# Kernel tuning notes

Hardware: AMD Instinct MI355X
Metric: run time of the kernel (lower is better)

Reference implementation:

```python
import jax, jax.numpy as jnp
import numpy as np

IMG = 640.0  # nominal image size for box coordinates
EPS_IOU = 1e-9   # eps used by iou_calculator
EPS_OVL = 1e-6   # eps used by bbox_overlaps


def _make_boxes(key, lead_shape):
    # Build valid <x1,y1,x2,y2> boxes: random centers in [0, IMG), sizes in [4, 204).
    k1, k2 = jax.random.split(key)
    c = jax.random.uniform(k1, lead_shape + (2,), dtype=jnp.float32) * IMG
    wh = jax.random.uniform(k2, lead_shape + (2,), dtype=jnp.float32) * 200.0 + 4.0
    return jnp.concatenate([c - wh / 2.0, c + wh / 2.0], axis=-1)


def setup_inputs() -> dict:
    key = jax.random.key(0)
    ka, kb, kc = jax.random.split(key, 3)
    gt_bboxes = _make_boxes(ka, (16, 128))        # (bs, n_max_boxes, 4)
    pred_bboxes = _make_boxes(kb, (16, 8400))     # (bs, num_total_anchors, 4)
    anchor_bboxes = _make_boxes(kc, (8400,))      # (num_total_anchors, 4)
    return {"gt_bboxes": gt_bboxes, "pred_bboxes": pred_bboxes, "anchor_bboxes": anchor_bboxes}


def _dist_calculator(gt_flat, anchor_bboxes):
    # gt_flat: (bs*M, 4), anchor_bboxes: (N, 4) -> distances (bs*M, N), ac_points (N, 2)
    gt_pts = (gt_flat[:, :2] + gt_flat[:, 2:]) / 2.0
    ac_pts = (anchor_bboxes[:, :2] + anchor_bboxes[:, 2:]) / 2.0
    d = jnp.sqrt(jnp.sum((gt_pts[:, None, :] - ac_pts[None, :, :]) ** 2, axis=-1))
    return d, ac_pts


def _iou_calculator(box1, box2, eps=EPS_IOU):
    # box1: (bs, M, 4), box2: (bs, N, 4) -> (bs, M, N) pairwise IoU
    b1 = box1[:, :, None, :]
    b2 = box2[:, None, :, :]
    lt = jnp.maximum(b1[..., :2], b2[..., :2])
    rb = jnp.minimum(b1[..., 2:], b2[..., 2:])
    wh = jnp.clip(rb - lt, 0.0)
    overlap = wh[..., 0] * wh[..., 1]
    area1 = (b1[..., 2] - b1[..., 0]) * (b1[..., 3] - b1[..., 1])
    area2 = (b2[..., 2] - b2[..., 0]) * (b2[..., 3] - b2[..., 1])
    union = area1 + area2 - overlap + eps
    return overlap / union


def _bbox_overlaps_giou(b1, b2, eps=EPS_OVL):
    # b1: (M, 4), b2: (N, 4) -> (M, N) pairwise GIoU (bbox_overlaps, mode='giou', is_aligned=False)
    area1 = (b1[:, 2] - b1[:, 0]) * (b1[:, 3] - b1[:, 1])
    area2 = (b2[:, 2] - b2[:, 0]) * (b2[:, 3] - b2[:, 1])
    lt = jnp.maximum(b1[:, None, :2], b2[None, :, :2])
    rb = jnp.minimum(b1[:, None, 2:], b2[None, :, 2:])
    wh = jnp.clip(rb - lt, 0.0)
    overlap = wh[..., 0] * wh[..., 1]
    union = jnp.maximum(area1[:, None] + area2[None, :] - overlap, eps)
    ious = overlap / union
    enclosed_lt = jnp.minimum(b1[:, None, :2], b2[None, :, :2])
    enclosed_rb = jnp.maximum(b1[:, None, 2:], b2[None, :, 2:])
    enclose_wh = jnp.clip(enclosed_rb - enclosed_lt, 0.0)
    enclose_area = jnp.maximum(enclose_wh[..., 0] * enclose_wh[..., 1], eps)
    return ious - (enclose_area - union) / enclose_area


def reference(gt_bboxes, pred_bboxes, anchor_bboxes):
    bs, M, _ = gt_bboxes.shape
    gt_flat = gt_bboxes.reshape(bs * M, 4)
    # ATSS assigner stage: center distance gt<->anchor and gt<->anchor GIoU
    distances, ac_points = _dist_calculator(gt_flat, anchor_bboxes)
    gious = _bbox_overlaps_giou(gt_flat, anchor_bboxes)
    # TAL assigner stage: batched pairwise IoU gt<->pred
    overlaps = _iou_calculator(gt_bboxes, pred_bboxes)
    return distances, overlaps, gious
```

## Files before the change

### kernel.cpp

```cpp
#include <hip/hip_runtime.h>


#define EPS_IOU 1e-9f
#define EPS_OVL 1e-6f

__device__ __forceinline__ void dist_giou(const float4 gb, float gcx, float gcy, float garea,
                                          const float4 ab, float& d, float& giou) {
    float acx = (ab.x + ab.z) * 0.5f;
    float acy = (ab.y + ab.w) * 0.5f;
    float dx = gcx - acx, dy = gcy - acy;
    d = sqrtf(dx * dx + dy * dy);
    float aarea = (ab.z - ab.x) * (ab.w - ab.y);
    float ltx = fmaxf(gb.x, ab.x), lty = fmaxf(gb.y, ab.y);
    float rbx = fminf(gb.z, ab.z), rby = fminf(gb.w, ab.w);
    float w = fmaxf(rbx - ltx, 0.0f), h = fmaxf(rby - lty, 0.0f);
    float overlap = w * h;
    float uni = fmaxf(garea + aarea - overlap, EPS_OVL);
    float iou = overlap / uni;
    float elx = fminf(gb.x, ab.x), ely = fminf(gb.y, ab.y);
    float erx = fmaxf(gb.z, ab.z), ery = fmaxf(gb.w, ab.w);
    float ew = fmaxf(erx - elx, 0.0f), eh = fmaxf(ery - ely, 0.0f);
    float earea = fmaxf(ew * eh, EPS_OVL);
    giou = iou - (earea - uni) / earea;
}

__device__ __forceinline__ float pred_iou(const float4 gb, float garea, const float4 pb) {
    float parea = (pb.z - pb.x) * (pb.w - pb.y);
    float ltx = fmaxf(gb.x, pb.x), lty = fmaxf(gb.y, pb.y);
    float rbx = fminf(gb.z, pb.z), rby = fminf(gb.w, pb.w);
    float w = fmaxf(rbx - ltx, 0.0f), h = fmaxf(rby - lty, 0.0f);
    float overlap = w * h;
    float uni = garea + parea - overlap + EPS_IOU;
    return overlap / uni;
}

__global__ __launch_bounds__(256) void yolov6_fused(
    const float4* __restrict__ gt,
    const float4* __restrict__ pred,
    const float4* __restrict__ anc,
    float* __restrict__ out_dist,
    float* __restrict__ out_ovl,
    float* __restrict__ out_giou,
    int N, int M)
{
    const int g = blockIdx.y;
    const int b = g / M;
    const int j4 = blockIdx.x * blockDim.x + threadIdx.x;
    const int j = j4 * 4;
    if (j >= N) return;

    const float4 gb = gt[g];
    const float gcx = (gb.x + gb.z) * 0.5f;
    const float gcy = (gb.y + gb.w) * 0.5f;
    const float garea = (gb.z - gb.x) * (gb.w - gb.y);

    const long long row = (long long)g * N;
    const float4* ancp = anc + j;
    const float4* predp = pred + (long long)b * N + j;

    if (j + 3 < N) {
        float dv[4], ov[4], gv[4];
#pragma unroll
        for (int k = 0; k < 4; ++k) {
            const float4 ab = ancp[k];
            dist_giou(gb, gcx, gcy, garea, ab, dv[k], gv[k]);
            const float4 pb = predp[k];
            ov[k] = pred_iou(gb, garea, pb);
        }
        *(float4*)(out_dist + row + j) = make_float4(dv[0], dv[1], dv[2], dv[3]);
        *(float4*)(out_ovl  + row + j) = make_float4(ov[0], ov[1], ov[2], ov[3]);
        *(float4*)(out_giou + row + j) = make_float4(gv[0], gv[1], gv[2], gv[3]);
    } else {
        for (int k = 0; j + k < N; ++k) {
            const float4 ab = ancp[k];
            float d, gi;
            dist_giou(gb, gcx, gcy, garea, ab, d, gi);
            const float4 pb = predp[k];
            float io = pred_iou(gb, garea, pb);
            out_dist[row + j + k] = d;
            out_ovl [row + j + k] = io;
            out_giou[row + j + k] = gi;
        }
    }
}

extern "C" void kernel_launch(void* const* d_in, const int* in_sizes, int n_in,
                              void* d_out, int out_size, void* d_ws, size_t ws_size,
                              hipStream_t stream) {
    const float4* gt   = (const float4*)d_in[0];
    const float4* pred = (const float4*)d_in[1];
    const float4* anc  = (const float4*)d_in[2];

    const int N  = in_sizes[2] / 4;
    const int bs = in_sizes[1] / in_sizes[2];
    const int GM = in_sizes[0] / 4;
    const int M  = GM / bs;

    float* out = (float*)d_out;
    const long long plane = (long long)GM * N;
    float* out_dist = out;
    float* out_ovl  = out + plane;
    float* out_giou = out + 2 * plane;

    const int cols = (N + 3) / 4;
    dim3 block(256);
    dim3 grid((cols + 255) / 256, GM);
    yolov6_fused<<<grid, block, 0, stream>>>(gt, pred, anc,
                                             out_dist, out_ovl, out_giou, N, M);
}
```

Baseline: 225.4 us.

## Process four gt rows per thread and use fast hardware rcp/sqrt

Each thread now loads its four anchor and pred boxes once and reuses them, along with their precomputed centers and areas, across four consecutive gt rows, so the grid's y-dimension shrinks by four. IEEE divisions and sqrt are replaced with the AMDGPU approximate rcp and sqrt builtins. The tail path for N not divisible by 4 is removed, and the code assumes GM divisible by ROWS and that the rows never straddle a batch boundary. The approximate reciprocal can change results slightly. The kernel is dominated by output writes (about 258 MB), so the saving on compute and loads may be small.

```diff
diff --git a/kernel.cpp b/kernel.cpp
--- a/kernel.cpp
+++ b/kernel.cpp
@@ -3,36 +3,10 @@
 
 #define EPS_IOU 1e-9f
 #define EPS_OVL 1e-6f
+#define ROWS 4
 
-__device__ __forceinline__ void dist_giou(const float4 gb, float gcx, float gcy, float garea,
-                                          const float4 ab, float& d, float& giou) {
-    float acx = (ab.x + ab.z) * 0.5f;
-    float acy = (ab.y + ab.w) * 0.5f;
-    float dx = gcx - acx, dy = gcy - acy;
-    d = sqrtf(dx * dx + dy * dy);
-    float aarea = (ab.z - ab.x) * (ab.w - ab.y);
-    float ltx = fmaxf(gb.x, ab.x), lty = fmaxf(gb.y, ab.y);
-    float rbx = fminf(gb.z, ab.z), rby = fminf(gb.w, ab.w);
-    float w = fmaxf(rbx - ltx, 0.0f), h = fmaxf(rby - lty, 0.0f);
-    float overlap = w * h;
-    float uni = fmaxf(garea + aarea - overlap, EPS_OVL);
-    float iou = overlap / uni;
-    float elx = fminf(gb.x, ab.x), ely = fminf(gb.y, ab.y);
-    float erx = fmaxf(gb.z, ab.z), ery = fmaxf(gb.w, ab.w);
-    float ew = fmaxf(erx - elx, 0.0f), eh = fmaxf(ery - ely, 0.0f);
-    float earea = fmaxf(ew * eh, EPS_OVL);
-    giou = iou - (earea - uni) / earea;
-}
-
-__device__ __forceinline__ float pred_iou(const float4 gb, float garea, const float4 pb) {
-    float parea = (pb.z - pb.x) * (pb.w - pb.y);
-    float ltx = fmaxf(gb.x, pb.x), lty = fmaxf(gb.y, pb.y);
-    float rbx = fminf(gb.z, pb.z), rby = fminf(gb.w, pb.w);
-    float w = fmaxf(rbx - ltx, 0.0f), h = fmaxf(rby - lty, 0.0f);
-    float overlap = w * h;
-    float uni = garea + parea - overlap + EPS_IOU;
-    return overlap / uni;
-}
+__device__ __forceinline__ float frcp(float x)  { return __builtin_amdgcn_rcpf(x); }
+__device__ __forceinline__ float fsqrtf_(float x){ return __builtin_amdgcn_sqrtf(x); }
 
 __global__ __launch_bounds__(256) void yolov6_fused(
     const float4* __restrict__ gt,
@@ -43,44 +17,63 @@
     float* __restrict__ out_giou,
     int N, int M)
 {
-    const int g = blockIdx.y;
-    const int b = g / M;
-    const int j4 = blockIdx.x * blockDim.x + threadIdx.x;
-    const int j = j4 * 4;
+    const int g0 = blockIdx.y * ROWS;
+    const int b  = g0 / M;
+    const int j  = (blockIdx.x * blockDim.x + threadIdx.x) * 4;
     if (j >= N) return;
 
-    const float4 gb = gt[g];
-    const float gcx = (gb.x + gb.z) * 0.5f;
-    const float gcy = (gb.y + gb.w) * 0.5f;
-    const float garea = (gb.z - gb.x) * (gb.w - gb.y);
+    float4 ab[4], pb[4];
+    float acx[4], acy[4], aarea[4], parea[4];
+    const float4* ancp  = anc + j;
+    const float4* predp = pred + (long long)b * N + j;
+#pragma unroll
+    for (int k = 0; k < 4; ++k) {
+        ab[k] = ancp[k];
+        pb[k] = predp[k];
+        acx[k]   = (ab[k].x + ab[k].z) * 0.5f;
+        acy[k]   = (ab[k].y + ab[k].w) * 0.5f;
+        aarea[k] = (ab[k].z - ab[k].x) * (ab[k].w - ab[k].y);
+        parea[k] = (pb[k].z - pb[k].x) * (pb[k].w - pb[k].y);
+    }
 
-    const long long row = (long long)g * N;
-    const float4* ancp = anc + j;
-    const float4* predp = pred + (long long)b * N + j;
+#pragma unroll
+    for (int r = 0; r < ROWS; ++r) {
+        const int g = g0 + r;
+        const float4 gb = gt[g];
+        const float gcx   = (gb.x + gb.z) * 0.5f;
+        const float gcy   = (gb.y + gb.w) * 0.5f;
+        const float garea = (gb.z - gb.x) * (gb.w - gb.y);
 
-    if (j + 3 < N) {
         float dv[4], ov[4], gv[4];
 #pragma unroll
         for (int k = 0; k < 4; ++k) {
-            const float4 ab = ancp[k];
-            dist_giou(gb, gcx, gcy, garea, ab, dv[k], gv[k]);
-            const float4 pb = predp[k];
-            ov[k] = pred_iou(gb, garea, pb);
+            float dx = gcx - acx[k], dy = gcy - acy[k];
+            dv[k] = fsqrtf_(dx * dx + dy * dy);
+            {
+                float ltx = fmaxf(gb.x, ab[k].x), lty = fmaxf(gb.y, ab[k].y);
+                float rbx = fminf(gb.z, ab[k].z), rby = fminf(gb.w, ab[k].w);
+                float w = fmaxf(rbx - ltx, 0.0f), h = fmaxf(rby - lty, 0.0f);
+                float overlap = w * h;
+                float uni = fmaxf(garea + aarea[k] - overlap, EPS_OVL);
+                float elx = fminf(gb.x, ab[k].x), ely = fminf(gb.y, ab[k].y);
+                float erx = fmaxf(gb.z, ab[k].z), ery = fmaxf(gb.w, ab[k].w);
+                float ew = fmaxf(erx - elx, 0.0f), eh = fmaxf(ery - ely, 0.0f);
+                float earea = fmaxf(ew * eh, EPS_OVL);
+                gv[k] = overlap * frcp(uni) - (earea - uni) * frcp(earea);
+            }
+            {
+                float ltx = fmaxf(gb.x, pb[k].x), lty = fmaxf(gb.y, pb[k].y);
+                float rbx = fminf(gb.z, pb[k].z), rby = fminf(gb.w, pb[k].w);
+                float w = fmaxf(rbx - ltx, 0.0f), h = fmaxf(rby - lty, 0.0f);
+                float overlap = w * h;
+                float uni = garea + parea[k] - overlap + EPS_IOU;
+                ov[k] = overlap * frcp(uni);
+            }
         }
-        *(float4*)(out_dist + row + j) = make_float4(dv[0], dv[1], dv[2], dv[3]);
-        *(float4*)(out_ovl  + row + j) = make_float4(ov[0], ov[1], ov[2], ov[3]);
-        *(float4*)(out_giou + row + j) = make_float4(gv[0], gv[1], gv[2], gv[3]);
-    } else {
-        for (int k = 0; j + k < N; ++k) {
-            const float4 ab = ancp[k];
-            float d, gi;
-            dist_giou(gb, gcx, gcy, garea, ab, d, gi);
-            const float4 pb = predp[k];
-            float io = pred_iou(gb, garea, pb);
-            out_dist[row + j + k] = d;
-            out_ovl [row + j + k] = io;
-            out_giou[row + j + k] = gi;
-        }
+        const long long row = (long long)g * N + j;
+        *(float4*)(out_dist + row) = make_float4(dv[0], dv[1], dv[2], dv[3]);
+        *(float4*)(out_ovl  + row) = make_float4(ov[0], ov[1], ov[2], ov[3]);
+        *(float4*)(out_giou + row) = make_float4(gv[0], gv[1], gv[2], gv[3]);
     }
 }
 
@@ -104,7 +97,7 @@
 
     const int cols = (N + 3) / 4;
     dim3 block(256);
-    dim3 grid((cols + 255) / 256, GM);
+    dim3 grid((cols + 255) / 256, GM / ROWS);
     yolov6_fused<<<grid, block, 0, stream>>>(gt, pred, anc,
                                              out_dist, out_ovl, out_giou, N, M);
 }
```

Result: faster. 204.6 us (-9.2%).
